# Kernel tuning notes

Hardware: AMD Instinct MI355X
Metric: run time of the kernel (lower is better)

Reference implementation:

```python
import jax, jax.numpy as jnp
import numpy as np

B, T, D_MODEL = 2, 1024, 1024
H, DEPTH = 8, 5
DH = D_MODEL // H


def setup_inputs() -> dict:
    key = jax.random.key(0)
    k_x, k_wp, k_bp, k_wv, k_wo = jax.random.split(key, 5)
    x = jax.random.normal(k_x, (B, T, D_MODEL), dtype=jnp.float32)
    # Parameters stored as [in, out] (y = x @ W + b), equivalent math to nn.Linear.
    Wp = jax.random.normal(k_wp, (D_MODEL, H * DEPTH), dtype=jnp.float32) * 0.02
    bp = jnp.zeros((H * DEPTH,), dtype=jnp.float32)
    Wv = jax.random.normal(k_wv, (D_MODEL, D_MODEL), dtype=jnp.float32) * 0.02
    Wo = jax.random.normal(k_wo, (D_MODEL, D_MODEL), dtype=jnp.float32) * 0.02
    return {"x": x, "Wp": Wp, "bp": bp, "Wv": Wv, "Wo": Wo}


def reference(x, Wp, bp, Wv, Wo):
    Bx, Tx, d = x.shape
    # soft binary path decisions: B,H,T,DEPTH
    paths = jax.nn.sigmoid(x @ Wp + bp)              # B,T,H*DEPTH
    paths = paths.reshape(Bx, Tx, H, DEPTH).transpose(0, 2, 1, 3)  # B,H,T,DEPTH
    # pairwise per-level agreement: B,H,Tq,Tk,DEPTH
    pq = paths[:, :, :, None, :]
    pk = paths[:, :, None, :, :]
    agree = pq * pk + (1.0 - pq) * (1.0 - pk)
    # shared-prefix length via cumprod over depth, summed
    sim = jnp.cumprod(agree, axis=-1).sum(axis=-1) / DEPTH  # B,H,Tq,Tk
    # causal mask
    mask = jnp.triu(jnp.ones((Tx, Tx), dtype=bool), k=1)
    sim = jnp.where(mask[None, None], -jnp.inf, sim)
    attn = jax.nn.softmax(sim, axis=-1)              # B,H,T,T
    V = (x @ Wv).reshape(Bx, Tx, H, DH).transpose(0, 2, 1, 3)  # B,H,T,dh
    ctx = jnp.einsum('bhqk,bhkd->bhqd', attn, V)
    ctx = ctx.transpose(0, 2, 1, 3).reshape(Bx, Tx, d)
    return ctx @ Wo
```

## Files before the change

kernel.cpp:

```cpp
#include <hip/hip_runtime.h>
#include <hip/hip_bf16.h>

#define B_ 2
#define T_ 1024
#define D_ 1024
#define H_ 8
#define DEPTH_ 5
#define DH_ 128

typedef short s16x8 __attribute__((ext_vector_type(8)));
typedef short s16x4 __attribute__((ext_vector_type(4)));
typedef float f32x4 __attribute__((ext_vector_type(4)));

__device__ inline short f2bf(float f) {
  __hip_bfloat16 h = __float2bfloat16(f);
  return *reinterpret_cast<short*>(&h);
}

__global__ __launch_bounds__(256) void transpose_convert2(
    const float* __restrict__ W0, const float* __restrict__ W1,
    short* __restrict__ T0, short* __restrict__ T1, int K, int N) {
  const float* W = blockIdx.z ? W1 : W0;
  short* Wt = blockIdx.z ? T1 : T0;
  __shared__ float tile[64][65];
  int k0 = blockIdx.y * 64, n0 = blockIdx.x * 64;
  int tid = threadIdx.x;
#pragma unroll
  for (int i = 0; i < 4; ++i) {
    int idx = tid + i * 256;
    int r = idx >> 4, c4 = (idx & 15) * 4;
    float4 v = *(const float4*)&W[(size_t)(k0 + r) * N + n0 + c4];
    tile[r][c4 + 0] = v.x;
    tile[r][c4 + 1] = v.y;
    tile[r][c4 + 2] = v.z;
    tile[r][c4 + 3] = v.w;
  }
  __syncthreads();
#pragma unroll
  for (int j = 0; j < 2; ++j) {
    int idx = tid + j * 256;
    int n = idx >> 3, k8 = (idx & 7) * 8;
    s16x8 outv;
#pragma unroll
    for (int jj = 0; jj < 8; ++jj) outv[jj] = f2bf(tile[k8 + jj][n]);
    *(s16x8*)&Wt[(size_t)(n0 + n) * K + k0 + k8] = outv;
  }
}

__global__ __launch_bounds__(256) void wp_transpose(
    const float* __restrict__ Wp, short* __restrict__ WBt) {
  int idx = blockIdx.x * 256 + threadIdx.x;
  int row = idx >> 7;
  int k8 = (idx & 127) * 8;
  s16x8 v;
  if (row < H_ * DEPTH_) {
#pragma unroll
    for (int j = 0; j < 8; ++j)
      v[j] = f2bf(Wp[(size_t)(k8 + j) * (H_ * DEPTH_) + row]);
  } else {
#pragma unroll
    for (int j = 0; j < 8; ++j) v[j] = 0;
  }
  *(s16x8*)&WBt[(size_t)(1024 + row) * D_ + k8] = v;
}

#define LS 72
__global__ __launch_bounds__(256) void gemm_x(
    const float* __restrict__ x, const short* __restrict__ WBt,
    const float* __restrict__ bp, short* __restrict__ Vt,
    float* __restrict__ paths_t) {
  __shared__ short As[64 * LS];
  __shared__ short Bs[64 * LS];
  int tid = threadIdx.x;
  int bm = blockIdx.y << 6, bn = blockIdx.x << 6;
  int wave = tid >> 6, lane = tid & 63;
  int wm = (wave >> 1) * 32, wn = (wave & 1) * 32;
  f32x4 acc[2][2] = {{{0.f, 0.f, 0.f, 0.f}, {0.f, 0.f, 0.f, 0.f}},
                     {{0.f, 0.f, 0.f, 0.f}, {0.f, 0.f, 0.f, 0.f}}};
  const int K = D_;

  for (int k0 = 0; k0 < K; k0 += 64) {
    s16x8 av[2], bv[2];
#pragma unroll
    for (int i = 0; i < 2; ++i) {
      int c = tid + i * 256;
      int row = c >> 3, ko = (c & 7) * 8;
      const float* p = &x[(size_t)(bm + row) * K + k0 + ko];
      float4 f0 = *(const float4*)p;
      float4 f1 = *(const float4*)(p + 4);
      av[i][0] = f2bf(f0.x); av[i][1] = f2bf(f0.y);
      av[i][2] = f2bf(f0.z); av[i][3] = f2bf(f0.w);
      av[i][4] = f2bf(f1.x); av[i][5] = f2bf(f1.y);
      av[i][6] = f2bf(f1.z); av[i][7] = f2bf(f1.w);
      bv[i] = *(const s16x8*)&WBt[(size_t)(bn + row) * K + k0 + ko];
    }
    __syncthreads();
#pragma unroll
    for (int i = 0; i < 2; ++i) {
      int c = tid + i * 256;
      int row = c >> 3, ko = (c & 7) * 8;
      *(s16x8*)&As[row * LS + ko] = av[i];
      *(s16x8*)&Bs[row * LS + ko] = bv[i];
    }
    __syncthreads();
#pragma unroll
    for (int ks = 0; ks < 2; ++ks) {
      int ko = ks * 32 + (lane >> 4) * 8;
      int fr = lane & 15;
      s16x8 a0 = *(const s16x8*)&As[(wm + fr) * LS + ko];
      s16x8 a1 = *(const s16x8*)&As[(wm + 16 + fr) * LS + ko];
      s16x8 b0 = *(const s16x8*)&Bs[(wn + fr) * LS + ko];
      s16x8 b1 = *(const s16x8*)&Bs[(wn + 16 + fr) * LS + ko];
      acc[0][0] = __builtin_amdgcn_mfma_f32_16x16x32_bf16(a0, b0, acc[0][0], 0, 0, 0);
      acc[0][1] = __builtin_amdgcn_mfma_f32_16x16x32_bf16(a0, b1, acc[0][1], 0, 0, 0);
      acc[1][0] = __builtin_amdgcn_mfma_f32_16x16x32_bf16(a1, b0, acc[1][0], 0, 0, 0);
      acc[1][1] = __builtin_amdgcn_mfma_f32_16x16x32_bf16(a1, b1, acc[1][1], 0, 0, 0);
    }
  }
  int col = lane & 15, rbase = (lane >> 4) * 4;
  if (bn < 1024) {
#pragma unroll
    for (int mi = 0; mi < 2; ++mi)
#pragma unroll
      for (int ni = 0; ni < 2; ++ni) {
        int m = bm + wm + mi * 16 + rbase;
        int n = bn + wn + ni * 16 + col;
        int b = m >> 10, t = m & (T_ - 1);
        int h = n >> 7, dh = n & (DH_ - 1);
        s16x4 v4;
#pragma unroll
        for (int r = 0; r < 4; ++r) v4[r] = f2bf(acc[mi][ni][r]);
        *(s16x4*)&Vt[((size_t)((b * H_ + h) * DH_ + dh)) * T_ + t] = v4;
      }
  } else {
#pragma unroll
    for (int ni = 0; ni < 2; ++ni) {
      int pn = wn + ni * 16 + col;
      if (pn < H_ * DEPTH_) {
        float bias = bp[pn];
        int h = pn / DEPTH_, d = pn % DEPTH_;
#pragma unroll
        for (int mi = 0; mi < 2; ++mi)
#pragma unroll
          for (int r = 0; r < 4; ++r) {
            int m = bm + wm + mi * 16 + rbase + r;
            int b = m >> 10, t = m & (T_ - 1);
            float p = 1.f / (1.f + __expf(-(acc[mi][ni][r] + bias)));
            paths_t[(((size_t)(b * H_ + h) * T_ + t) * DEPTH_) + d] = p;
          }
      }
    }
  }
}

__global__ __launch_bounds__(256) void gemm_out(
    const short* __restrict__ Ab, const short* __restrict__ Bt,
    float* __restrict__ C, int M, int N, int K) {
  __shared__ short As[64 * LS];
  __shared__ short Bs[64 * LS];
  int tid = threadIdx.x;
  int bm = blockIdx.y << 6, bn = blockIdx.x << 6;
  int wave = tid >> 6, lane = tid & 63;
  int wm = (wave >> 1) * 32, wn = (wave & 1) * 32;
  f32x4 acc[2][2] = {{{0.f, 0.f, 0.f, 0.f}, {0.f, 0.f, 0.f, 0.f}},
                     {{0.f, 0.f, 0.f, 0.f}, {0.f, 0.f, 0.f, 0.f}}};

  for (int k0 = 0; k0 < K; k0 += 64) {
    s16x8 av[2], bv[2];
#pragma unroll
    for (int i = 0; i < 2; ++i) {
      int c = tid + i * 256;
      int row = c >> 3, ko = (c & 7) * 8;
      av[i] = *(const s16x8*)&Ab[(size_t)(bm + row) * K + k0 + ko];
      bv[i] = *(const s16x8*)&Bt[(size_t)(bn + row) * K + k0 + ko];
    }
    __syncthreads();
#pragma unroll
    for (int i = 0; i < 2; ++i) {
      int c = tid + i * 256;
      int row = c >> 3, ko = (c & 7) * 8;
      *(s16x8*)&As[row * LS + ko] = av[i];
      *(s16x8*)&Bs[row * LS + ko] = bv[i];
    }
    __syncthreads();
#pragma unroll
    for (int ks = 0; ks < 2; ++ks) {
      int ko = ks * 32 + (lane >> 4) * 8;
      int fr = lane & 15;
      s16x8 a0 = *(const s16x8*)&As[(wm + fr) * LS + ko];
      s16x8 a1 = *(const s16x8*)&As[(wm + 16 + fr) * LS + ko];
      s16x8 b0 = *(const s16x8*)&Bs[(wn + fr) * LS + ko];
      s16x8 b1 = *(const s16x8*)&Bs[(wn + 16 + fr) * LS + ko];
      acc[0][0] = __builtin_amdgcn_mfma_f32_16x16x32_bf16(a0, b0, acc[0][0], 0, 0, 0);
      acc[0][1] = __builtin_amdgcn_mfma_f32_16x16x32_bf16(a0, b1, acc[0][1], 0, 0, 0);
      acc[1][0] = __builtin_amdgcn_mfma_f32_16x16x32_bf16(a1, b0, acc[1][0], 0, 0, 0);
      acc[1][1] = __builtin_amdgcn_mfma_f32_16x16x32_bf16(a1, b1, acc[1][1], 0, 0, 0);
    }
  }
  int col = lane & 15, rbase = (lane >> 4) * 4;
#pragma unroll
  for (int mi = 0; mi < 2; ++mi)
#pragma unroll
    for (int ni = 0; ni < 2; ++ni)
#pragma unroll
      for (int r = 0; r < 4; ++r)
        C[(size_t)(bm + wm + mi * 16 + rbase + r) * N + bn + wn + ni * 16 +
          col] = acc[mi][ni][r];
}

#define QT 32
#define KT 64

__global__ __launch_bounds__(256) void attn_kernel(
    const float* __restrict__ paths_t, const short* __restrict__ Vt,
    short* __restrict__ ctxb) {
  int bh = blockIdx.y;
  int b = bh >> 3, h = bh & 7;
  int bx = blockIdx.x;
  int wave = threadIdx.x >> 6, lane = threadIdx.x & 63;

  __shared__ short Vs[DH_ * LS];
  __shared__ short Ss[QT * LS];
  __shared__ float lsum_s[QT];

  const float* pb = paths_t + (size_t)bh * T_ * DEPTH_;
  const short* vb = Vt + (size_t)bh * DH_ * T_;

  for (int half = 0; half < 2; ++half) {
    int qt = half ? (31 - bx) : bx;
    int q0 = qt * QT;
    int nkt = (q0 + QT - 1) / KT + 1;

    float pq[8][DEPTH_], mq[8][DEPTH_];
#pragma unroll
    for (int j = 0; j < 8; ++j) {
      const float* qr = pb + (size_t)(q0 + wave * 8 + j) * DEPTH_;
#pragma unroll
      for (int d = 0; d < DEPTH_; ++d) {
        pq[j][d] = qr[d];
        mq[j][d] = 1.f - pq[j][d];
      }
    }
    f32x4 acc[2][2] = {{{0.f, 0.f, 0.f, 0.f}, {0.f, 0.f, 0.f, 0.f}},
                       {{0.f, 0.f, 0.f, 0.f}, {0.f, 0.f, 0.f, 0.f}}};
    float part[8] = {};

    for (int kt = 0; kt < nkt; ++kt) {
      int k0 = kt * KT;
      __syncthreads();
#pragma unroll
      for (int i = 0; i < 4; ++i) {
        int c = threadIdx.x + i * 256;
        int dh = c >> 3, ko = (c & 7) * 8;
        *(s16x8*)&Vs[dh * LS + ko] =
            *(const s16x8*)&vb[(size_t)dh * T_ + k0 + ko];
      }
      int kg = k0 + lane;
      const float* kr = pb + (size_t)kg * DEPTH_;
      float pk[DEPTH_], mk[DEPTH_];
#pragma unroll
      for (int d = 0; d < DEPTH_; ++d) {
        pk[d] = kr[d];
        mk[d] = 1.f - pk[d];
      }
#pragma unroll
      for (int j = 0; j < 8; ++j) {
        int qg = q0 + wave * 8 + j;
        float a0 = fmaf(pq[j][0], pk[0], mq[j][0] * mk[0]);
        float a1 = fmaf(pq[j][1], pk[1], mq[j][1] * mk[1]);
        float a2 = fmaf(pq[j][2], pk[2], mq[j][2] * mk[2]);
        float a3 = fmaf(pq[j][3], pk[3], mq[j][3] * mk[3]);
        float a4 = fmaf(pq[j][4], pk[4], mq[j][4] * mk[4]);
        float t4 = 1.f + a4;
        float t3 = fmaf(a3, t4, 1.f);
        float t2 = fmaf(a2, t3, 1.f);
        float t1 = fmaf(a1, t2, 1.f);
        float s = a0 * t1;
        float w = (kg <= qg) ? __expf(s * 0.2f) : 0.f;
        part[j] += w;
        Ss[(wave * 8 + j) * LS + lane] = f2bf(w);
      }
      __syncthreads();
#pragma unroll
      for (int ks = 0; ks < 2; ++ks) {
        int ko = ks * 32 + (lane >> 4) * 8;
        int fr = lane & 15;
        s16x8 sa0 = *(const s16x8*)&Ss[fr * LS + ko];
        s16x8 sa1 = *(const s16x8*)&Ss[(16 + fr) * LS + ko];
        s16x8 vb0 = *(const s16x8*)&Vs[(wave * 32 + fr) * LS + ko];
        s16x8 vb1 = *(const s16x8*)&Vs[(wave * 32 + 16 + fr) * LS + ko];
        acc[0][0] = __builtin_amdgcn_mfma_f32_16x16x32_bf16(sa0, vb0, acc[0][0], 0, 0, 0);
        acc[0][1] = __builtin_amdgcn_mfma_f32_16x16x32_bf16(sa0, vb1, acc[0][1], 0, 0, 0);
        acc[1][0] = __builtin_amdgcn_mfma_f32_16x16x32_bf16(sa1, vb0, acc[1][0], 0, 0, 0);
        acc[1][1] = __builtin_amdgcn_mfma_f32_16x16x32_bf16(sa1, vb1, acc[1][1], 0, 0, 0);
      }
    }
#pragma unroll
    for (int j = 0; j < 8; ++j) {
      float s = part[j];
#pragma unroll
      for (int off = 32; off >= 1; off >>= 1) s += __shfl_xor(s, off, 64);
      if (lane == j) lsum_s[wave * 8 + j] = s;
    }
    __syncthreads();
    int col = lane & 15, rbase = (lane >> 4) * 4;
#pragma unroll
    for (int qt2 = 0; qt2 < 2; ++qt2)
#pragma unroll
      for (int ni = 0; ni < 2; ++ni)
#pragma unroll
        for (int r = 0; r < 4; ++r) {
          int ql = qt2 * 16 + rbase + r;
          int dh = wave * 32 + ni * 16 + col;
          float val = acc[qt2][ni][r] / lsum_s[ql];
          ctxb[(size_t)(b * T_ + q0 + ql) * D_ + h * DH_ + dh] = f2bf(val);
        }
  }
}

extern "C" void kernel_launch(void* const* d_in, const int* in_sizes, int n_in,
                              void* d_out, int out_size, void* d_ws,
                              size_t ws_size, hipStream_t stream) {
  const float* x = (const float*)d_in[0];
  const float* Wp = (const float*)d_in[1];
  const float* bp = (const float*)d_in[2];
  const float* Wv = (const float*)d_in[3];
  const float* Wo = (const float*)d_in[4];
  float* out = (float*)d_out;

  char* ws = (char*)d_ws;
  float* paths_t = (float*)ws;
  short* Vt = (short*)(ws + 327680);
  short* WBt = (short*)(ws + 327680 + 4194304);
  short* Wot = (short*)(ws + 327680 + 4194304 + 2228224);
  short* ctxb = (short*)(ws + 327680 + 4194304 + 2228224 + 2097152);

  transpose_convert2<<<dim3(16, 16, 2), 256, 0, stream>>>(Wv, Wo, WBt, Wot,
                                                          D_, D_);
  wp_transpose<<<dim3(32), 256, 0, stream>>>(Wp, WBt);
  gemm_x<<<dim3(17, B_ * T_ / 64), 256, 0, stream>>>(x, WBt, bp, Vt, paths_t);
  attn_kernel<<<dim3(16, B_ * H_), 256, 0, stream>>>(paths_t, Vt, ctxb);
  gemm_out<<<dim3(D_ / 64, B_ * T_ / 64), 256, 0, stream>>>(ctxb, Wot, out,
                                                            B_ * T_, D_, D_);
}
```

Before: 135.7 us.

## Merge prep kernels, use direct global-to-LDS loads with XOR swizzle, widen attention blocks

```diff
diff --git a/kernel.cpp b/kernel.cpp
--- a/kernel.cpp
+++ b/kernel.cpp
@@ -17,100 +17,119 @@
   return *reinterpret_cast<short*>(&h);
 }
 
-__global__ __launch_bounds__(256) void transpose_convert2(
-    const float* __restrict__ W0, const float* __restrict__ W1,
-    short* __restrict__ T0, short* __restrict__ T1, int K, int N) {
-  const float* W = blockIdx.z ? W1 : W0;
-  short* Wt = blockIdx.z ? T1 : T0;
-  __shared__ float tile[64][65];
-  int k0 = blockIdx.y * 64, n0 = blockIdx.x * 64;
+typedef __attribute__((address_space(3))) unsigned int lds_u32_t;
+typedef __attribute__((address_space(1))) unsigned int glb_u32_t;
+__device__ __forceinline__ void glds16(const void* g, void* l) {
+  __builtin_amdgcn_global_load_lds((const glb_u32_t*)g, (lds_u32_t*)l, 16, 0,
+                                   0);
+}
+
+__global__ __launch_bounds__(256) void prep_kernel(
+    const float* __restrict__ Wv, const float* __restrict__ Wo,
+    const float* __restrict__ Wp, const float* __restrict__ x,
+    short* __restrict__ WBt, short* __restrict__ Wot,
+    short* __restrict__ xb) {
   int tid = threadIdx.x;
-#pragma unroll
-  for (int i = 0; i < 4; ++i) {
-    int idx = tid + i * 256;
-    int r = idx >> 4, c4 = (idx & 15) * 4;
-    float4 v = *(const float4*)&W[(size_t)(k0 + r) * N + n0 + c4];
-    tile[r][c4 + 0] = v.x;
-    tile[r][c4 + 1] = v.y;
-    tile[r][c4 + 2] = v.z;
-    tile[r][c4 + 3] = v.w;
+  if (blockIdx.z < 2) {
+    const float* W = blockIdx.z ? Wo : Wv;
+    short* Wt = blockIdx.z ? Wot : WBt;
+    __shared__ float tile[64][65];
+    int k0 = blockIdx.y * 64, n0 = blockIdx.x * 64;
+#pragma unroll
+    for (int i = 0; i < 4; ++i) {
+      int idx = tid + i * 256;
+      int r = idx >> 4, c4 = (idx & 15) * 4;
+      float4 v = *(const float4*)&W[(size_t)(k0 + r) * D_ + n0 + c4];
+      tile[r][c4 + 0] = v.x;
+      tile[r][c4 + 1] = v.y;
+      tile[r][c4 + 2] = v.z;
+      tile[r][c4 + 3] = v.w;
+    }
+    __syncthreads();
+#pragma unroll
+    for (int j = 0; j < 2; ++j) {
+      int idx = tid + j * 256;
+      int n = idx >> 3, k8 = (idx & 7) * 8;
+      s16x8 outv;
+#pragma unroll
+      for (int jj = 0; jj < 8; ++jj) outv[jj] = f2bf(tile[k8 + jj][n]);
+      *(s16x8*)&Wt[(size_t)(n0 + n) * D_ + k0 + k8] = outv;
+    }
+  } else {
+    int bid = blockIdx.y * 16 + blockIdx.x;
+#pragma unroll
+    for (int c = 0; c < 4; ++c) {
+      size_t idx = (size_t)bid * 8192 + c * 2048 + tid * 8;
+      float4 f0 = *(const float4*)&x[idx];
+      float4 f1 = *(const float4*)&x[idx + 4];
+      s16x8 v;
+      v[0] = f2bf(f0.x); v[1] = f2bf(f0.y);
+      v[2] = f2bf(f0.z); v[3] = f2bf(f0.w);
+      v[4] = f2bf(f1.x); v[5] = f2bf(f1.y);
+      v[6] = f2bf(f1.z); v[7] = f2bf(f1.w);
+      *(s16x8*)&xb[idx] = v;
+    }
+    if (bid < 4) {
+#pragma unroll
+      for (int it = 0; it < 8; ++it) {
+        int item = bid * 2048 + it * 256 + tid;
+        int row = item >> 7, k8 = (item & 127) * 8;
+        s16x8 v;
+        if (row < H_ * DEPTH_) {
+#pragma unroll
+          for (int j = 0; j < 8; ++j)
+            v[j] = f2bf(Wp[(size_t)(k8 + j) * (H_ * DEPTH_) + row]);
+        } else {
+#pragma unroll
+          for (int j = 0; j < 8; ++j) v[j] = 0;
+        }
+        *(s16x8*)&WBt[(size_t)(1024 + row) * D_ + k8] = v;
+      }
+    }
   }
-  __syncthreads();
-#pragma unroll
-  for (int j = 0; j < 2; ++j) {
-    int idx = tid + j * 256;
-    int n = idx >> 3, k8 = (idx & 7) * 8;
-    s16x8 outv;
-#pragma unroll
-    for (int jj = 0; jj < 8; ++jj) outv[jj] = f2bf(tile[k8 + jj][n]);
-    *(s16x8*)&Wt[(size_t)(n0 + n) * K + k0 + k8] = outv;
-  }
-}
-
-__global__ __launch_bounds__(256) void wp_transpose(
-    const float* __restrict__ Wp, short* __restrict__ WBt) {
-  int idx = blockIdx.x * 256 + threadIdx.x;
-  int row = idx >> 7;
-  int k8 = (idx & 127) * 8;
-  s16x8 v;
-  if (row < H_ * DEPTH_) {
-#pragma unroll
-    for (int j = 0; j < 8; ++j)
-      v[j] = f2bf(Wp[(size_t)(k8 + j) * (H_ * DEPTH_) + row]);
-  } else {
-#pragma unroll
-    for (int j = 0; j < 8; ++j) v[j] = 0;
-  }
-  *(s16x8*)&WBt[(size_t)(1024 + row) * D_ + k8] = v;
-}
-
-#define LS 72
-__global__ __launch_bounds__(256) void gemm_x(
-    const float* __restrict__ x, const short* __restrict__ WBt,
-    const float* __restrict__ bp, short* __restrict__ Vt,
-    float* __restrict__ paths_t) {
-  __shared__ short As[64 * LS];
-  __shared__ short Bs[64 * LS];
+}
+
+template <int MODE>
+__global__ __launch_bounds__(256) void gemm64(
+    const short* __restrict__ A, const short* __restrict__ Bt,
+    float* __restrict__ Cf, const float* __restrict__ bp,
+    short* __restrict__ Vt, float* __restrict__ paths_t) {
+  __shared__ short As[64 * 64];
+  __shared__ short Bs[64 * 64];
+  const int K = D_;
   int tid = threadIdx.x;
   int bm = blockIdx.y << 6, bn = blockIdx.x << 6;
-  int wave = tid >> 6, lane = tid & 63;
-  int wm = (wave >> 1) * 32, wn = (wave & 1) * 32;
+  int w = tid >> 6, lane = tid & 63;
+  int wm = (w >> 1) * 32, wn = (w & 1) * 32;
+  int g = lane >> 4, fr = lane & 15, frx = fr & 7;
+  int srow = lane >> 3;
+  int scol = ((lane & 7) ^ srow) * 8;
   f32x4 acc[2][2] = {{{0.f, 0.f, 0.f, 0.f}, {0.f, 0.f, 0.f, 0.f}},
                      {{0.f, 0.f, 0.f, 0.f}, {0.f, 0.f, 0.f, 0.f}}};
-  const int K = D_;
+
+  const short* Ar0 = A + (size_t)(bm + w * 8 + srow) * K + scol;
+  const short* Ar1 = A + (size_t)(bm + 32 + w * 8 + srow) * K + scol;
+  const short* Br0 = Bt + (size_t)(bn + w * 8 + srow) * K + scol;
+  const short* Br1 = Bt + (size_t)(bn + 32 + w * 8 + srow) * K + scol;
+  short* lA0 = &As[(w * 8) * 64];
+  short* lA1 = &As[(32 + w * 8) * 64];
+  short* lB0 = &Bs[(w * 8) * 64];
+  short* lB1 = &Bs[(32 + w * 8) * 64];
 
   for (int k0 = 0; k0 < K; k0 += 64) {
-    s16x8 av[2], bv[2];
-#pragma unroll
-    for (int i = 0; i < 2; ++i) {
-      int c = tid + i * 256;
-      int row = c >> 3, ko = (c & 7) * 8;
-      const float* p = &x[(size_t)(bm + row) * K + k0 + ko];
-      float4 f0 = *(const float4*)p;
-      float4 f1 = *(const float4*)(p + 4);
-      av[i][0] = f2bf(f0.x); av[i][1] = f2bf(f0.y);
-      av[i][2] = f2bf(f0.z); av[i][3] = f2bf(f0.w);
-      av[i][4] = f2bf(f1.x); av[i][5] = f2bf(f1.y);
-      av[i][6] = f2bf(f1.z); av[i][7] = f2bf(f1.w);
-      bv[i] = *(const s16x8*)&WBt[(size_t)(bn + row) * K + k0 + ko];
-    }
     __syncthreads();
-#pragma unroll
-    for (int i = 0; i < 2; ++i) {
-      int c = tid + i * 256;
-      int row = c >> 3, ko = (c & 7) * 8;
-      *(s16x8*)&As[row * LS + ko] = av[i];
-      *(s16x8*)&Bs[row * LS + ko] = bv[i];
-    }
+    glds16(Ar0 + k0, lA0);
+    glds16(Ar1 + k0, lA1);
+    glds16(Br0 + k0, lB0);
+    glds16(Br1 + k0, lB1);
     __syncthreads();
 #pragma unroll
     for (int ks = 0; ks < 2; ++ks) {
-      int ko = ks * 32 + (lane >> 4) * 8;
-      int fr = lane & 15;
-      s16x8 a0 = *(const s16x8*)&As[(wm + fr) * LS + ko];
-      s16x8 a1 = *(const s16x8*)&As[(wm + 16 + fr) * LS + ko];
-      s16x8 b0 = *(const s16x8*)&Bs[(wn + fr) * LS + ko];
-      s16x8 b1 = *(const s16x8*)&Bs[(wn + 16 + fr) * LS + ko];
+      int sl = ((ks * 4 + g) ^ frx) * 8;
+      s16x8 a0 = *(const s16x8*)&As[(wm + fr) * 64 + sl];
+      s16x8 a1 = *(const s16x8*)&As[(wm + 16 + fr) * 64 + sl];
+      s16x8 b0 = *(const s16x8*)&Bs[(wn + fr) * 64 + sl];
+      s16x8 b1 = *(const s16x8*)&Bs[(wn + 16 + fr) * 64 + sl];
       acc[0][0] = __builtin_amdgcn_mfma_f32_16x16x32_bf16(a0, b0, acc[0][0], 0, 0, 0);
       acc[0][1] = __builtin_amdgcn_mfma_f32_16x16x32_bf16(a0, b1, acc[0][1], 0, 0, 0);
       acc[1][0] = __builtin_amdgcn_mfma_f32_16x16x32_bf16(a1, b0, acc[1][0], 0, 0, 0);
@@ -118,7 +137,16 @@
     }
   }
   int col = lane & 15, rbase = (lane >> 4) * 4;
-  if (bn < 1024) {
+  if (MODE == 0) {
+#pragma unroll
+    for (int mi = 0; mi < 2; ++mi)
+#pragma unroll
+      for (int ni = 0; ni < 2; ++ni)
+#pragma unroll
+        for (int r = 0; r < 4; ++r)
+          Cf[(size_t)(bm + wm + mi * 16 + rbase + r) * D_ + bn + wn +
+             ni * 16 + col] = acc[mi][ni][r];
+  } else if (bn < 1024) {
 #pragma unroll
     for (int mi = 0; mi < 2; ++mi)
 #pragma unroll
@@ -153,104 +181,48 @@
   }
 }
 
-__global__ __launch_bounds__(256) void gemm_out(
-    const short* __restrict__ Ab, const short* __restrict__ Bt,
-    float* __restrict__ C, int M, int N, int K) {
-  __shared__ short As[64 * LS];
-  __shared__ short Bs[64 * LS];
-  int tid = threadIdx.x;
-  int bm = blockIdx.y << 6, bn = blockIdx.x << 6;
-  int wave = tid >> 6, lane = tid & 63;
-  int wm = (wave >> 1) * 32, wn = (wave & 1) * 32;
-  f32x4 acc[2][2] = {{{0.f, 0.f, 0.f, 0.f}, {0.f, 0.f, 0.f, 0.f}},
-                     {{0.f, 0.f, 0.f, 0.f}, {0.f, 0.f, 0.f, 0.f}}};
-
-  for (int k0 = 0; k0 < K; k0 += 64) {
-    s16x8 av[2], bv[2];
-#pragma unroll
-    for (int i = 0; i < 2; ++i) {
-      int c = tid + i * 256;
-      int row = c >> 3, ko = (c & 7) * 8;
-      av[i] = *(const s16x8*)&Ab[(size_t)(bm + row) * K + k0 + ko];
-      bv[i] = *(const s16x8*)&Bt[(size_t)(bn + row) * K + k0 + ko];
-    }
-    __syncthreads();
-#pragma unroll
-    for (int i = 0; i < 2; ++i) {
-      int c = tid + i * 256;
-      int row = c >> 3, ko = (c & 7) * 8;
-      *(s16x8*)&As[row * LS + ko] = av[i];
-      *(s16x8*)&Bs[row * LS + ko] = bv[i];
-    }
-    __syncthreads();
-#pragma unroll
-    for (int ks = 0; ks < 2; ++ks) {
-      int ko = ks * 32 + (lane >> 4) * 8;
-      int fr = lane & 15;
-      s16x8 a0 = *(const s16x8*)&As[(wm + fr) * LS + ko];
-      s16x8 a1 = *(const s16x8*)&As[(wm + 16 + fr) * LS + ko];
-      s16x8 b0 = *(const s16x8*)&Bs[(wn + fr) * LS + ko];
-      s16x8 b1 = *(const s16x8*)&Bs[(wn + 16 + fr) * LS + ko];
-      acc[0][0] = __builtin_amdgcn_mfma_f32_16x16x32_bf16(a0, b0, acc[0][0], 0, 0, 0);
-      acc[0][1] = __builtin_amdgcn_mfma_f32_16x16x32_bf16(a0, b1, acc[0][1], 0, 0, 0);
-      acc[1][0] = __builtin_amdgcn_mfma_f32_16x16x32_bf16(a1, b0, acc[1][0], 0, 0, 0);
-      acc[1][1] = __builtin_amdgcn_mfma_f32_16x16x32_bf16(a1, b1, acc[1][1], 0, 0, 0);
-    }
-  }
-  int col = lane & 15, rbase = (lane >> 4) * 4;
-#pragma unroll
-  for (int mi = 0; mi < 2; ++mi)
-#pragma unroll
-    for (int ni = 0; ni < 2; ++ni)
-#pragma unroll
-      for (int r = 0; r < 4; ++r)
-        C[(size_t)(bm + wm + mi * 16 + rbase + r) * N + bn + wn + ni * 16 +
-          col] = acc[mi][ni][r];
-}
-
-#define QT 32
-#define KT 64
-
-__global__ __launch_bounds__(256) void attn_kernel(
+#define LS 72
+
+__global__ __launch_bounds__(512) void attn_kernel(
     const float* __restrict__ paths_t, const short* __restrict__ Vt,
     short* __restrict__ ctxb) {
   int bh = blockIdx.y;
   int b = bh >> 3, h = bh & 7;
   int bx = blockIdx.x;
-  int wave = threadIdx.x >> 6, lane = threadIdx.x & 63;
+  int w = threadIdx.x >> 6, lane = threadIdx.x & 63;
+  int g = lane >> 4, fr = lane & 15;
 
   __shared__ short Vs[DH_ * LS];
-  __shared__ short Ss[QT * LS];
-  __shared__ float lsum_s[QT];
+  __shared__ short Ss[32 * LS];
+  __shared__ float lsum_s[32];
 
   const float* pb = paths_t + (size_t)bh * T_ * DEPTH_;
   const short* vb = Vt + (size_t)bh * DH_ * T_;
 
   for (int half = 0; half < 2; ++half) {
     int qt = half ? (31 - bx) : bx;
-    int q0 = qt * QT;
-    int nkt = (q0 + QT - 1) / KT + 1;
-
-    float pq[8][DEPTH_], mq[8][DEPTH_];
-#pragma unroll
-    for (int j = 0; j < 8; ++j) {
-      const float* qr = pb + (size_t)(q0 + wave * 8 + j) * DEPTH_;
+    int q0 = qt * 32;
+    int nkt = q0 / 64 + 1;
+
+    float pq[4][DEPTH_], mq[4][DEPTH_];
+#pragma unroll
+    for (int j = 0; j < 4; ++j) {
+      const float* qr = pb + (size_t)(q0 + w * 4 + j) * DEPTH_;
 #pragma unroll
       for (int d = 0; d < DEPTH_; ++d) {
         pq[j][d] = qr[d];
         mq[j][d] = 1.f - pq[j][d];
       }
     }
-    f32x4 acc[2][2] = {{{0.f, 0.f, 0.f, 0.f}, {0.f, 0.f, 0.f, 0.f}},
-                       {{0.f, 0.f, 0.f, 0.f}, {0.f, 0.f, 0.f, 0.f}}};
-    float part[8] = {};
+    f32x4 acc[2] = {{0.f, 0.f, 0.f, 0.f}, {0.f, 0.f, 0.f, 0.f}};
+    float part[4] = {};
 
     for (int kt = 0; kt < nkt; ++kt) {
-      int k0 = kt * KT;
+      int k0 = kt * 64;
       __syncthreads();
 #pragma unroll
-      for (int i = 0; i < 4; ++i) {
-        int c = threadIdx.x + i * 256;
+      for (int i = 0; i < 2; ++i) {
+        int c = threadIdx.x + i * 512;
         int dh = c >> 3, ko = (c & 7) * 8;
         *(s16x8*)&Vs[dh * LS + ko] =
             *(const s16x8*)&vb[(size_t)dh * T_ + k0 + ko];
@@ -264,8 +236,8 @@
         mk[d] = 1.f - pk[d];
       }
 #pragma unroll
-      for (int j = 0; j < 8; ++j) {
-        int qg = q0 + wave * 8 + j;
+      for (int j = 0; j < 4; ++j) {
+        int qg = q0 + w * 4 + j;
         float a0 = fmaf(pq[j][0], pk[0], mq[j][0] * mk[0]);
         float a1 = fmaf(pq[j][1], pk[1], mq[j][1] * mk[1]);
         float a2 = fmaf(pq[j][2], pk[2], mq[j][2] * mk[2]);
@@ -276,45 +248,39 @@
         float t2 = fmaf(a2, t3, 1.f);
         float t1 = fmaf(a1, t2, 1.f);
         float s = a0 * t1;
-        float w = (kg <= qg) ? __expf(s * 0.2f) : 0.f;
-        part[j] += w;
-        Ss[(wave * 8 + j) * LS + lane] = f2bf(w);
+        float wv = (kg <= qg) ? __expf(s * 0.2f) : 0.f;
+        part[j] += wv;
+        Ss[(w * 4 + j) * LS + lane] = f2bf(wv);
       }
       __syncthreads();
 #pragma unroll
       for (int ks = 0; ks < 2; ++ks) {
-        int ko = ks * 32 + (lane >> 4) * 8;
-        int fr = lane & 15;
+        int ko = ks * 32 + g * 8;
         s16x8 sa0 = *(const s16x8*)&Ss[fr * LS + ko];
         s16x8 sa1 = *(const s16x8*)&Ss[(16 + fr) * LS + ko];
-        s16x8 vb0 = *(const s16x8*)&Vs[(wave * 32 + fr) * LS + ko];
-        s16x8 vb1 = *(const s16x8*)&Vs[(wave * 32 + 16 + fr) * LS + ko];
-        acc[0][0] = __builtin_amdgcn_mfma_f32_16x16x32_bf16(sa0, vb0, acc[0][0], 0, 0, 0);
-        acc[0][1] = __builtin_amdgcn_mfma_f32_16x16x32_bf16(sa0, vb1, acc[0][1], 0, 0, 0);
-        acc[1][0] = __builtin_amdgcn_mfma_f32_16x16x32_bf16(sa1, vb0, acc[1][0], 0, 0, 0);
-        acc[1][1] = __builtin_amdgcn_mfma_f32_16x16x32_bf16(sa1, vb1, acc[1][1], 0, 0, 0);
-      }
-    }
-#pragma unroll
-    for (int j = 0; j < 8; ++j) {
+        s16x8 vv = *(const s16x8*)&Vs[(w * 16 + fr) * LS + ko];
+        acc[0] = __builtin_amdgcn_mfma_f32_16x16x32_bf16(sa0, vv, acc[0], 0, 0, 0);
+        acc[1] = __builtin_amdgcn_mfma_f32_16x16x32_bf16(sa1, vv, acc[1], 0, 0, 0);
+      }
+    }
+#pragma unroll
+    for (int j = 0; j < 4; ++j) {
       float s = part[j];
 #pragma unroll
       for (int off = 32; off >= 1; off >>= 1) s += __shfl_xor(s, off, 64);
-      if (lane == j) lsum_s[wave * 8 + j] = s;
+      if (lane == j) lsum_s[w * 4 + j] = s;
     }
     __syncthreads();
-    int col = lane & 15, rbase = (lane >> 4) * 4;
+    int col = lane & 15, rbase = g * 4;
 #pragma unroll
     for (int qt2 = 0; qt2 < 2; ++qt2)
 #pragma unroll
-      for (int ni = 0; ni < 2; ++ni)
-#pragma unroll
-        for (int r = 0; r < 4; ++r) {
-          int ql = qt2 * 16 + rbase + r;
-          int dh = wave * 32 + ni * 16 + col;
-          float val = acc[qt2][ni][r] / lsum_s[ql];
-          ctxb[(size_t)(b * T_ + q0 + ql) * D_ + h * DH_ + dh] = f2bf(val);
-        }
+      for (int r = 0; r < 4; ++r) {
+        int ql = qt2 * 16 + rbase + r;
+        int dh = w * 16 + col;
+        float val = acc[qt2][r] / lsum_s[ql];
+        ctxb[(size_t)(b * T_ + q0 + ql) * D_ + h * DH_ + dh] = f2bf(val);
+      }
   }
 }
 
@@ -331,15 +297,16 @@
   char* ws = (char*)d_ws;
   float* paths_t = (float*)ws;
   short* Vt = (short*)(ws + 327680);
-  short* WBt = (short*)(ws + 327680 + 4194304);
-  short* Wot = (short*)(ws + 327680 + 4194304 + 2228224);
-  short* ctxb = (short*)(ws + 327680 + 4194304 + 2228224 + 2097152);
-
-  transpose_convert2<<<dim3(16, 16, 2), 256, 0, stream>>>(Wv, Wo, WBt, Wot,
-                                                          D_, D_);
-  wp_transpose<<<dim3(32), 256, 0, stream>>>(Wp, WBt);
-  gemm_x<<<dim3(17, B_ * T_ / 64), 256, 0, stream>>>(x, WBt, bp, Vt, paths_t);
-  attn_kernel<<<dim3(16, B_ * H_), 256, 0, stream>>>(paths_t, Vt, ctxb);
-  gemm_out<<<dim3(D_ / 64, B_ * T_ / 64), 256, 0, stream>>>(ctxb, Wot, out,
-                                                            B_ * T_, D_, D_);
-}
+  short* WBt = (short*)(ws + 4521984);
+  short* Wot = (short*)(ws + 6750208);
+  short* ctxb = (short*)(ws + 8847360);
+  short* xb = (short*)(ws + 13041664);
+
+  prep_kernel<<<dim3(16, 16, 3), 256, 0, stream>>>(Wv, Wo, Wp, x, WBt, Wot,
+                                                   xb);
+  gemm64<1><<<dim3(17, 32), 256, 0, stream>>>(xb, WBt, nullptr, bp, Vt,
+                                              paths_t);
+  attn_kernel<<<dim3(16, B_ * H_), 512, 0, stream>>>(paths_t, Vt, ctxb);
+  gemm64<0><<<dim3(16, 32), 256, 0, stream>>>(ctxb, Wot, out, nullptr,
+                                              nullptr, nullptr);
+}
```

New measurement: 128.9 us. -5.0%, faster.
